# Kernel optimization log

Measured on AMD Instinct MI355X. Metric: run time of the kernel, lower is better.

## Reference

```python
import jax, jax.numpy as jnp
import numpy as np

B, T, D = 32, 1024, 512
G, K = 8, 256          # num_groups, codes_per_group
GD = D // G            # group_dim = 64


def setup_inputs() -> dict:
    key = jax.random.key(0)
    k_x, k_cb = jax.random.split(key)
    x = jax.random.normal(k_x, (B, T, D), dtype=jnp.float32)
    # nn.Embedding weights init uniform_(-1/K, 1/K), one table per group -> [G, K, GD]
    codebooks = jax.random.uniform(k_cb, (G, K, GD), dtype=jnp.float32,
                                   minval=-1.0 / K, maxval=1.0 / K)
    return {"x": x, "codebooks": codebooks}


def reference(x, codebooks):
    Bx, Tx, Dx = x.shape
    xg = x.reshape(Bx, Tx, G, GD)                      # [B,T,G,gd]
    # squared euclidean distances to each code, per group: [B,T,G,K]
    x_sq = jnp.sum(xg ** 2, axis=-1, keepdims=True)    # [B,T,G,1]
    c_sq = jnp.sum(codebooks ** 2, axis=-1)            # [G,K]
    xc = jnp.einsum('btgd,gkd->btgk', xg, codebooks)   # [B,T,G,K]
    d = x_sq + c_sq[None, None] - 2.0 * xc
    idx = jnp.argmin(d, axis=-1)                       # [B,T,G] int
    # gather selected codes: codebooks[g, idx[b,t,g]] -> [B,T,G,gd]
    xq = jnp.take_along_axis(codebooks[None, None],    # [1,1,G,K,gd]
                             idx[..., None, None], axis=3).squeeze(3)
    sg = jax.lax.stop_gradient
    # per-group mse means (over B,T,gd), summed over groups (matches torch loop)
    losses = (jnp.sum(jnp.mean((sg(xq) - xg) ** 2, axis=(0, 1, 3)))
              + jnp.sum(jnp.mean((xq - sg(xg)) ** 2, axis=(0, 1, 3))))
    # straight-through estimator
    xq_st = xg + sg(xq - xg)
    x_q = xq_st.reshape(Bx, Tx, Dx)
    return x_q, losses, idx
```

## Files before the change

### kernel.cpp

```cpp
#include <hip/hip_runtime.h>

#define BT_TOTAL (32 * 1024)
#define DIM 512
#define NG 8
#define NK 256
#define GD 64
#define QB 128

#define XQ_ELEMS (BT_TOTAL * DIM)
#define LOSS_OFF XQ_ELEMS
#define IDX_OFF (XQ_ELEMS + 1)

typedef float f32x16 __attribute__((ext_vector_type(16)));

__global__ void pq_prep(const float* __restrict__ cb,
                        float* __restrict__ csq,
                        float* __restrict__ loss_slot) {
    int i = blockIdx.x * 256 + threadIdx.x;
    if (i == 0) *loss_slot = 0.0f;
    if (i < NG * NK) {
        const float* row = cb + (size_t)i * GD;
        float a0 = 0.f, a1 = 0.f, a2 = 0.f, a3 = 0.f;
#pragma unroll
        for (int d = 0; d < GD; d += 4) {
            a0 = fmaf(row[d + 0], row[d + 0], a0);
            a1 = fmaf(row[d + 1], row[d + 1], a1);
            a2 = fmaf(row[d + 2], row[d + 2], a2);
            a3 = fmaf(row[d + 3], row[d + 3], a3);
        }
        csq[i] = (a0 + a1) + (a2 + a3);
    }
}

__global__ __launch_bounds__(256)
void pq_main(const float* __restrict__ x,
             const float* __restrict__ cb,
             const float* __restrict__ csq,
             float* __restrict__ out) {
    const int g = blockIdx.y;
    const int t = threadIdx.x;
    const int kh = __builtin_amdgcn_readfirstlane(t >> 7);
    const int ql = t & (QB - 1);
    const int q0 = blockIdx.x * QB;
    const int bt = q0 + ql;

    __shared__ float m_d[QB];
    __shared__ int   m_i[QB];
    __shared__ float wsum[4];

    const float* cbg = cb + (size_t)g * NK * GD;
    const float* csqg = csq + g * NK;

    const float* xrow = x + (size_t)bt * DIM + g * GD;
    float xr[64];
#pragma unroll
    for (int i = 0; i < 16; ++i) {
        float4 v = ((const float4*)xrow)[i];
        xr[i * 4 + 0] = v.x;
        xr[i * 4 + 1] = v.y;
        xr[i * 4 + 2] = v.z;
        xr[i * 4 + 3] = v.w;
    }

    float a0 = 0.f, a1 = 0.f, a2 = 0.f, a3 = 0.f;
#pragma unroll
    for (int i = 0; i < 16; ++i) {
        a0 = fmaf(xr[i * 4 + 0], xr[i * 4 + 0], a0);
        a1 = fmaf(xr[i * 4 + 1], xr[i * 4 + 1], a1);
        a2 = fmaf(xr[i * 4 + 2], xr[i * 4 + 2], a2);
        a3 = fmaf(xr[i * 4 + 3], xr[i * 4 + 3], a3);
    }
    const float x_sq = (a0 + a1) + (a2 + a3);

    const int kbase = kh << 7;
    float best = 3.402823466e38f;
    int bi = kbase;

#pragma unroll 1
    for (int kk = 0; kk < NK / 2; ++kk) {
        const int k = kbase + kk;
        f32x16 c0, c1, c2, c3;
        float cs;
        const float* ck = cbg + (size_t)k * GD;
        const float* pk = csqg + k;
        asm volatile(
            "s_load_dwordx16 %0, %5, 0x0\n\t"
            "s_load_dwordx16 %1, %5, 0x40\n\t"
            "s_load_dwordx16 %2, %5, 0x80\n\t"
            "s_load_dwordx16 %3, %5, 0xc0\n\t"
            "s_load_dword    %4, %6, 0x0"
            : "=s"(c0), "=s"(c1), "=s"(c2), "=s"(c3), "=s"(cs)
            : "s"(ck), "s"(pk));
        asm volatile("s_waitcnt lgkmcnt(0)"
                     : "+s"(c0), "+s"(c1), "+s"(c2), "+s"(c3), "+s"(cs));

        float d0 = 0.f, d1 = 0.f, d2 = 0.f, d3 = 0.f;
#define Q4(cv, i4, b)                                     \
        d0 = fmaf(cv[(i4) * 4 + 0], xr[(b) * 4 + 0], d0); \
        d1 = fmaf(cv[(i4) * 4 + 1], xr[(b) * 4 + 1], d1); \
        d2 = fmaf(cv[(i4) * 4 + 2], xr[(b) * 4 + 2], d2); \
        d3 = fmaf(cv[(i4) * 4 + 3], xr[(b) * 4 + 3], d3);
        Q4(c0, 0, 0)  Q4(c0, 1, 1)  Q4(c0, 2, 2)  Q4(c0, 3, 3)
        Q4(c1, 0, 4)  Q4(c1, 1, 5)  Q4(c1, 2, 6)  Q4(c1, 3, 7)
        Q4(c2, 0, 8)  Q4(c2, 1, 9)  Q4(c2, 2, 10) Q4(c2, 3, 11)
        Q4(c3, 0, 12) Q4(c3, 1, 13) Q4(c3, 2, 14) Q4(c3, 3, 15)
#undef Q4
        float dot = (d0 + d1) + (d2 + d3);
        float dist = (x_sq + cs) - 2.0f * dot;
        if (dist < best) { best = dist; bi = k; }
    }

    if (kh == 1) { m_d[ql] = best; m_i[ql] = bi; }
    __syncthreads();
    if (kh == 0) {
        float dh = m_d[ql];
        int ih = m_i[ql];
        if (dh < best) { best = dh; bi = ih; }
        m_i[ql] = bi;
        out[IDX_OFF + (size_t)bt * NG + g] = (float)bi;
    }
    __syncthreads();

    const int r_off = t >> 4;
    const int c4i = t & 15;
    float s0 = 0.f, s1 = 0.f, s2 = 0.f, s3 = 0.f;
#pragma unroll
    for (int p = 0; p < 8; ++p) {
        const int r = p * 16 + r_off;
        const int code = m_i[r];
        const size_t base = (size_t)(q0 + r) * DIM + g * GD + c4i * 4;
        float4 x4 = *(const float4*)(x + base);
        float4 q4 = *(const float4*)(cbg + (size_t)code * GD + c4i * 4);
        float dx = q4.x - x4.x;
        float dy = q4.y - x4.y;
        float dz = q4.z - x4.z;
        float dw = q4.w - x4.w;
        float4 o;
        o.x = x4.x + dx;
        o.y = x4.y + dy;
        o.z = x4.z + dz;
        o.w = x4.w + dw;
        *(float4*)(out + base) = o;
        s0 = fmaf(dx, dx, s0);
        s1 = fmaf(dy, dy, s1);
        s2 = fmaf(dz, dz, s2);
        s3 = fmaf(dw, dw, s3);
    }
    float part = (s0 + s1) + (s2 + s3);

#pragma unroll
    for (int off = 32; off > 0; off >>= 1) part += __shfl_down(part, off);

    const int lane = t & 63;
    const int wid = t >> 6;
    if (lane == 0) wsum[wid] = part;
    __syncthreads();
    if (t == 0) {
        float bs = (wsum[0] + wsum[1]) + (wsum[2] + wsum[3]);
        atomicAdd(out + LOSS_OFF, bs * (2.0f / 2097152.0f));
    }
}

extern "C" void kernel_launch(void* const* d_in, const int* in_sizes, int n_in,
                              void* d_out, int out_size, void* d_ws, size_t ws_size,
                              hipStream_t stream) {
    const float* x = (const float*)d_in[0];
    const float* cb = (const float*)d_in[1];
    float* out = (float*)d_out;
    float* csq = (float*)d_ws;

    pq_prep<<<dim3(8), dim3(256), 0, stream>>>(cb, csq, out + LOSS_OFF);

    dim3 grid(BT_TOTAL / QB, NG);
    pq_main<<<grid, dim3(256), 0, stream>>>(x, cb, csq, out);
}
```

Before: 124.9 us.

## Double-buffer codebook rows in VGPRs and use packed FMA for dot products

Codebook rows are no longer fetched with inline scalar loads followed by a full lgkmcnt wait. Each row is now loaded into vector registers, and the next row is prefetched while the current one is being consumed. The dot product is computed with two-wide packed FMAs (v_pk_fma_f32) to halve the FMA instruction count. The codebook addresses are uniform across the wave, so these loads likely still go through the vector memory path as broadcasts. That adds VGPR pressure (64 x values plus 128 for the buffers) and may lower occupancy.

```diff
diff --git a/kernel.cpp b/kernel.cpp
--- a/kernel.cpp
+++ b/kernel.cpp
@@ -11,7 +11,7 @@
 #define LOSS_OFF XQ_ELEMS
 #define IDX_OFF (XQ_ELEMS + 1)
 
-typedef float f32x16 __attribute__((ext_vector_type(16)));
+typedef float f32x2 __attribute__((ext_vector_type(2)));
 
 __global__ void pq_prep(const float* __restrict__ cb,
                         float* __restrict__ csq,
@@ -72,42 +72,48 @@
     }
     const float x_sq = (a0 + a1) + (a2 + a3);
 
+#pragma unroll
+    for (int i = 0; i < 64; ++i) asm("" : "+v"(xr[i]));
+
     const int kbase = kh << 7;
     float best = 3.402823466e38f;
     int bi = kbase;
 
+    float4 rc[16];
+    {
+        const float4* c4 = (const float4*)(cbg + (size_t)kbase * GD);
+#pragma unroll
+        for (int j = 0; j < 16; ++j) rc[j] = c4[j];
+    }
+
 #pragma unroll 1
     for (int kk = 0; kk < NK / 2; ++kk) {
         const int k = kbase + kk;
-        f32x16 c0, c1, c2, c3;
-        float cs;
-        const float* ck = cbg + (size_t)k * GD;
-        const float* pk = csqg + k;
-        asm volatile(
-            "s_load_dwordx16 %0, %5, 0x0\n\t"
-            "s_load_dwordx16 %1, %5, 0x40\n\t"
-            "s_load_dwordx16 %2, %5, 0x80\n\t"
-            "s_load_dwordx16 %3, %5, 0xc0\n\t"
-            "s_load_dword    %4, %6, 0x0"
-            : "=s"(c0), "=s"(c1), "=s"(c2), "=s"(c3), "=s"(cs)
-            : "s"(ck), "s"(pk));
-        asm volatile("s_waitcnt lgkmcnt(0)"
-                     : "+s"(c0), "+s"(c1), "+s"(c2), "+s"(c3), "+s"(cs));
+        const int knext = (kk < NK / 2 - 1) ? (k + 1) : kbase;
+        const float4* c4n = (const float4*)(cbg + (size_t)knext * GD);
+        float4 rn[16];
+#pragma unroll
+        for (int j = 0; j < 16; ++j) rn[j] = c4n[j];
 
-        float d0 = 0.f, d1 = 0.f, d2 = 0.f, d3 = 0.f;
-#define Q4(cv, i4, b)                                     \
-        d0 = fmaf(cv[(i4) * 4 + 0], xr[(b) * 4 + 0], d0); \
-        d1 = fmaf(cv[(i4) * 4 + 1], xr[(b) * 4 + 1], d1); \
-        d2 = fmaf(cv[(i4) * 4 + 2], xr[(b) * 4 + 2], d2); \
-        d3 = fmaf(cv[(i4) * 4 + 3], xr[(b) * 4 + 3], d3);
-        Q4(c0, 0, 0)  Q4(c0, 1, 1)  Q4(c0, 2, 2)  Q4(c0, 3, 3)
-        Q4(c1, 0, 4)  Q4(c1, 1, 5)  Q4(c1, 2, 6)  Q4(c1, 3, 7)
-        Q4(c2, 0, 8)  Q4(c2, 1, 9)  Q4(c2, 2, 10) Q4(c2, 3, 11)
-        Q4(c3, 0, 12) Q4(c3, 1, 13) Q4(c3, 2, 14) Q4(c3, 3, 15)
-#undef Q4
-        float dot = (d0 + d1) + (d2 + d3);
+        const float cs = csqg[k];
+
+        f32x2 acc01 = (f32x2){0.f, 0.f};
+        f32x2 acc23 = (f32x2){0.f, 0.f};
+#pragma unroll
+        for (int i = 0; i < 16; ++i) {
+            acc01 = __builtin_elementwise_fma(
+                (f32x2){rc[i].x, rc[i].y},
+                (f32x2){xr[i * 4 + 0], xr[i * 4 + 1]}, acc01);
+            acc23 = __builtin_elementwise_fma(
+                (f32x2){rc[i].z, rc[i].w},
+                (f32x2){xr[i * 4 + 2], xr[i * 4 + 3]}, acc23);
+        }
+        float dot = (acc01.x + acc01.y) + (acc23.x + acc23.y);
         float dist = (x_sq + cs) - 2.0f * dot;
         if (dist < best) { best = dist; bi = k; }
+
+#pragma unroll
+        for (int j = 0; j < 16; ++j) rc[j] = rn[j];
     }
 
     if (kh == 1) { m_d[ql] = best; m_i[ql] = bi; }
```

New measurement: 135.7 us. 8.7% more time.

## Process two query rows per thread to reuse scalar-loaded codebook rows

Applied to the files above, without the earlier changes.

Each thread now holds two x rows (A and B) and computes distances for both against every codebook row it loads into scalar registers, so the block covers 256 queries instead of 128. Each scalar codebook load is reused for twice as many FMAs and the grid halves. The cost is roughly double the VGPRs for x data (128 floats), which lowers occupancy and could add spilling, and there are fewer blocks to hide s_load latency.

```diff
diff --git a/kernel.cpp b/kernel.cpp
--- a/kernel.cpp
+++ b/kernel.cpp
@@ -5,7 +5,7 @@
 #define NG 8
 #define NK 256
 #define GD 64
-#define QB 128
+#define QB 256
 
 #define XQ_ELEMS (BT_TOTAL * DIM)
 #define LOSS_OFF XQ_ELEMS
@@ -40,9 +40,10 @@
     const int g = blockIdx.y;
     const int t = threadIdx.x;
     const int kh = __builtin_amdgcn_readfirstlane(t >> 7);
-    const int ql = t & (QB - 1);
+    const int ql = t & 127;
     const int q0 = blockIdx.x * QB;
-    const int bt = q0 + ql;
+    const int btA = q0 + ql;
+    const int btB = q0 + 128 + ql;
 
     __shared__ float m_d[QB];
     __shared__ int   m_i[QB];
@@ -51,30 +52,47 @@
     const float* cbg = cb + (size_t)g * NK * GD;
     const float* csqg = csq + g * NK;
 
-    const float* xrow = x + (size_t)bt * DIM + g * GD;
-    float xr[64];
+    const float* xrowA = x + (size_t)btA * DIM + g * GD;
+    const float* xrowB = x + (size_t)btB * DIM + g * GD;
+    float xrA[64], xrB[64];
 #pragma unroll
     for (int i = 0; i < 16; ++i) {
-        float4 v = ((const float4*)xrow)[i];
-        xr[i * 4 + 0] = v.x;
-        xr[i * 4 + 1] = v.y;
-        xr[i * 4 + 2] = v.z;
-        xr[i * 4 + 3] = v.w;
-    }
-
-    float a0 = 0.f, a1 = 0.f, a2 = 0.f, a3 = 0.f;
+        float4 v = ((const float4*)xrowA)[i];
+        xrA[i * 4 + 0] = v.x; xrA[i * 4 + 1] = v.y;
+        xrA[i * 4 + 2] = v.z; xrA[i * 4 + 3] = v.w;
+    }
 #pragma unroll
     for (int i = 0; i < 16; ++i) {
-        a0 = fmaf(xr[i * 4 + 0], xr[i * 4 + 0], a0);
-        a1 = fmaf(xr[i * 4 + 1], xr[i * 4 + 1], a1);
-        a2 = fmaf(xr[i * 4 + 2], xr[i * 4 + 2], a2);
-        a3 = fmaf(xr[i * 4 + 3], xr[i * 4 + 3], a3);
-    }
-    const float x_sq = (a0 + a1) + (a2 + a3);
+        float4 v = ((const float4*)xrowB)[i];
+        xrB[i * 4 + 0] = v.x; xrB[i * 4 + 1] = v.y;
+        xrB[i * 4 + 2] = v.z; xrB[i * 4 + 3] = v.w;
+    }
+
+    float x_sqA, x_sqB;
+    {
+        float a0 = 0.f, a1 = 0.f, a2 = 0.f, a3 = 0.f;
+#pragma unroll
+        for (int i = 0; i < 16; ++i) {
+            a0 = fmaf(xrA[i * 4 + 0], xrA[i * 4 + 0], a0);
+            a1 = fmaf(xrA[i * 4 + 1], xrA[i * 4 + 1], a1);
+            a2 = fmaf(xrA[i * 4 + 2], xrA[i * 4 + 2], a2);
+            a3 = fmaf(xrA[i * 4 + 3], xrA[i * 4 + 3], a3);
+        }
+        x_sqA = (a0 + a1) + (a2 + a3);
+        float b0 = 0.f, b1 = 0.f, b2 = 0.f, b3 = 0.f;
+#pragma unroll
+        for (int i = 0; i < 16; ++i) {
+            b0 = fmaf(xrB[i * 4 + 0], xrB[i * 4 + 0], b0);
+            b1 = fmaf(xrB[i * 4 + 1], xrB[i * 4 + 1], b1);
+            b2 = fmaf(xrB[i * 4 + 2], xrB[i * 4 + 2], b2);
+            b3 = fmaf(xrB[i * 4 + 3], xrB[i * 4 + 3], b3);
+        }
+        x_sqB = (b0 + b1) + (b2 + b3);
+    }
 
     const int kbase = kh << 7;
-    float best = 3.402823466e38f;
-    int bi = kbase;
+    float bestA = 3.402823466e38f, bestB = 3.402823466e38f;
+    int biA = kbase, biB = kbase;
 
 #pragma unroll 1
     for (int kk = 0; kk < NK / 2; ++kk) {
@@ -94,30 +112,51 @@
         asm volatile("s_waitcnt lgkmcnt(0)"
                      : "+s"(c0), "+s"(c1), "+s"(c2), "+s"(c3), "+s"(cs));
 
-        float d0 = 0.f, d1 = 0.f, d2 = 0.f, d3 = 0.f;
-#define Q4(cv, i4, b)                                     \
-        d0 = fmaf(cv[(i4) * 4 + 0], xr[(b) * 4 + 0], d0); \
-        d1 = fmaf(cv[(i4) * 4 + 1], xr[(b) * 4 + 1], d1); \
-        d2 = fmaf(cv[(i4) * 4 + 2], xr[(b) * 4 + 2], d2); \
-        d3 = fmaf(cv[(i4) * 4 + 3], xr[(b) * 4 + 3], d3);
-        Q4(c0, 0, 0)  Q4(c0, 1, 1)  Q4(c0, 2, 2)  Q4(c0, 3, 3)
-        Q4(c1, 0, 4)  Q4(c1, 1, 5)  Q4(c1, 2, 6)  Q4(c1, 3, 7)
-        Q4(c2, 0, 8)  Q4(c2, 1, 9)  Q4(c2, 2, 10) Q4(c2, 3, 11)
-        Q4(c3, 0, 12) Q4(c3, 1, 13) Q4(c3, 2, 14) Q4(c3, 3, 15)
+#define Q4(cv, i4, b, xarr)                                 \
+        d0 = fmaf(cv[(i4) * 4 + 0], xarr[(b) * 4 + 0], d0); \
+        d1 = fmaf(cv[(i4) * 4 + 1], xarr[(b) * 4 + 1], d1); \
+        d2 = fmaf(cv[(i4) * 4 + 2], xarr[(b) * 4 + 2], d2); \
+        d3 = fmaf(cv[(i4) * 4 + 3], xarr[(b) * 4 + 3], d3);
+        {
+            float d0 = 0.f, d1 = 0.f, d2 = 0.f, d3 = 0.f;
+            Q4(c0, 0, 0, xrA)  Q4(c0, 1, 1, xrA)  Q4(c0, 2, 2, xrA)  Q4(c0, 3, 3, xrA)
+            Q4(c1, 0, 4, xrA)  Q4(c1, 1, 5, xrA)  Q4(c1, 2, 6, xrA)  Q4(c1, 3, 7, xrA)
+            Q4(c2, 0, 8, xrA)  Q4(c2, 1, 9, xrA)  Q4(c2, 2, 10, xrA) Q4(c2, 3, 11, xrA)
+            Q4(c3, 0, 12, xrA) Q4(c3, 1, 13, xrA) Q4(c3, 2, 14, xrA) Q4(c3, 3, 15, xrA)
+            float dot = (d0 + d1) + (d2 + d3);
+            float dist = (x_sqA + cs) - 2.0f * dot;
+            if (dist < bestA) { bestA = dist; biA = k; }
+        }
+        {
+            float d0 = 0.f, d1 = 0.f, d2 = 0.f, d3 = 0.f;
+            Q4(c0, 0, 0, xrB)  Q4(c0, 1, 1, xrB)  Q4(c0, 2, 2, xrB)  Q4(c0, 3, 3, xrB)
+            Q4(c1, 0, 4, xrB)  Q4(c1, 1, 5, xrB)  Q4(c1, 2, 6, xrB)  Q4(c1, 3, 7, xrB)
+            Q4(c2, 0, 8, xrB)  Q4(c2, 1, 9, xrB)  Q4(c2, 2, 10, xrB) Q4(c2, 3, 11, xrB)
+            Q4(c3, 0, 12, xrB) Q4(c3, 1, 13, xrB) Q4(c3, 2, 14, xrB) Q4(c3, 3, 15, xrB)
+            float dot = (d0 + d1) + (d2 + d3);
+            float dist = (x_sqB + cs) - 2.0f * dot;
+            if (dist < bestB) { bestB = dist; biB = k; }
+        }
 #undef Q4
-        float dot = (d0 + d1) + (d2 + d3);
-        float dist = (x_sq + cs) - 2.0f * dot;
-        if (dist < best) { best = dist; bi = k; }
-    }
-
-    if (kh == 1) { m_d[ql] = best; m_i[ql] = bi; }
+    }
+
+    if (kh == 1) {
+        m_d[ql] = bestA;       m_i[ql] = biA;
+        m_d[128 + ql] = bestB; m_i[128 + ql] = biB;
+    }
     __syncthreads();
     if (kh == 0) {
         float dh = m_d[ql];
         int ih = m_i[ql];
-        if (dh < best) { best = dh; bi = ih; }
-        m_i[ql] = bi;
-        out[IDX_OFF + (size_t)bt * NG + g] = (float)bi;
+        if (dh < bestA) { bestA = dh; biA = ih; }
+        m_i[ql] = biA;
+        out[IDX_OFF + (size_t)btA * NG + g] = (float)biA;
+
+        float dh2 = m_d[128 + ql];
+        int ih2 = m_i[128 + ql];
+        if (dh2 < bestB) { bestB = dh2; biB = ih2; }
+        m_i[128 + ql] = biB;
+        out[IDX_OFF + (size_t)btB * NG + g] = (float)biB;
     }
     __syncthreads();
 
@@ -125,7 +164,7 @@
     const int c4i = t & 15;
     float s0 = 0.f, s1 = 0.f, s2 = 0.f, s3 = 0.f;
 #pragma unroll
-    for (int p = 0; p < 8; ++p) {
+    for (int p = 0; p < 16; ++p) {
         const int r = p * 16 + r_off;
         const int code = m_i[r];
         const size_t base = (size_t)(q0 + r) * DIM + g * GD + c4i * 4;
```

Result: slower. 154.2 us (+23.5%).
